# Kernel optimization log

Measured on AMD Instinct MI355X. Metric: run time of the kernel, lower is better.

Reference implementation:

```python
import jax, jax.numpy as jnp
import numpy as np

N = 16384          # nodes
E_R = 524288       # radial edges (avg degree 32)
E_B = 32768        # bonded edges
N_TYPES = 20       # atom types
CS = 64            # scalar (0e) channels
CV = 32            # vector (1o) channels
EA = 16            # edge_attr_dim
EA_B = EA // 2     # bondedness embedding dim
EA_R = (EA + 1) // 2  # radial basis dim
CUTOFF = 1.5       # effective_radial_cutoff
L = 2              # n_layers
NORM = float(np.sqrt((E_R + E_B) / N))  # ~sqrt(avg degree) message normalization


def setup_inputs() -> dict:
    key = jax.random.key(0)
    ks = jax.random.split(key, 32)
    def rn(i, shape, scale=1.0):
        return jax.random.normal(ks[i], shape, dtype=jnp.float32) * scale
    s_e = 1.0 / np.sqrt(EA)
    inp = {}
    inp["pos"] = rn(0, (N, 3))
    inp["c_noise"] = rn(1, (1,))
    inp["atom_types"] = jax.random.randint(ks[2], (N,), 0, N_TYPES)
    inp["radial_edge_index"] = jax.random.randint(ks[3], (2, E_R), 0, N)
    inp["bonded_edge_index"] = jax.random.randint(ks[4], (2, E_B), 0, N)
    # learned parameters
    inp["atom_tab"] = rn(5, (N_TYPES, CS))
    inp["bond_tab"] = rn(6, (2, EA_B))
    inp["ns0_w"] = rn(7, (CS,), 0.1)
    inp["We0"] = rn(8, (EA, CS), s_e)
    inp["We1"] = rn(9, (EA, CS), s_e)
    inp["Wself0"] = rn(10, (CS, CS), 1.0 / np.sqrt(CS))
    inp["Ws0"] = rn(11, (CS, CS), 1.0 / np.sqrt(CS))
    inp["Wv0"] = rn(12, (CS, CV), 1.0 / np.sqrt(CS))
    inp["ns_w"] = rn(13, (L, CS + CV), 0.1)
    inp["We_ss"] = rn(14, (L, EA, CS), s_e)
    inp["We_vs"] = rn(15, (L, EA, CV), s_e)
    inp["We_sv"] = rn(16, (L, EA, CS), s_e)
    inp["We_vv"] = rn(17, (L, EA, CV), s_e)
    inp["We_vx"] = rn(18, (L, EA, CV), s_e)
    inp["Wmix_s"] = rn(19, (L, CS + CV, CS), 1.0 / np.sqrt(CS + CV))
    inp["Wmix_v"] = rn(20, (L, CS + 2 * CV, CV), 1.0 / np.sqrt(CS + 2 * CV))
    inp["Wself_s"] = rn(21, (L, CS, CS), 1.0 / np.sqrt(CS))
    inp["Wself_v"] = rn(22, (L, CV, CV), 1.0 / np.sqrt(CV))
    inp["skip_w"] = rn(23, (L, 2 * (CS + CV)), 0.1)
    inp["skip_b"] = rn(24, (L, 2 * (CS + CV)), 0.1)
    inp["w_out"] = rn(25, (CV,), 1.0 / np.sqrt(CV))
    inp["gain"] = jnp.asarray(0.5, dtype=jnp.float32)
    return inp


def _radial_basis(d):
    # e3nn soft_one_hot_linspace, basis='gaussian', cutoff=True
    centers = jnp.linspace(0.0, CUTOFF, EA_R + 2)[1:-1]
    step = centers[1] - centers[0]
    diff = (d[:, None] - centers[None, :]) / step
    return jnp.exp(-diff * diff) * 1.12


def reference(pos, c_noise, atom_tab, bond_tab, ns0_w, We0, We1, Wself0, Ws0, Wv0,
              ns_w, We_ss, We_vs, We_sv, We_vv, We_vx, Wmix_s, Wmix_v, Wself_s, Wself_v,
              skip_w, skip_b, w_out, gain, atom_types, radial_edge_index, bonded_edge_index):
    edge_index = jnp.concatenate([radial_edge_index, bonded_edge_index], axis=1)
    bond_mask = jnp.concatenate([jnp.zeros((E_R,), jnp.int32), jnp.ones((E_B,), jnp.int32)])
    src, dst = edge_index[0], edge_index[1]
    edge_vec = pos[src] - pos[dst]                      # [E,3]
    d = jnp.sqrt(jnp.sum(edge_vec * edge_vec, -1) + 1e-12)
    Y1 = jnp.sqrt(3.0) * edge_vec / d[:, None]          # l=1 SH, component norm; Y0 == 1
    edge_attr = jnp.concatenate([bond_tab[bond_mask], _radial_basis(d)], axis=-1)  # [E,EA]

    # atom embedding + initial noise-conditional scaling
    s = atom_tab[atom_types] * (1.0 + c_noise * ns0_w)  # [N,CS]

    # initial projector: scalar-input equivariant conv -> hidden irreps
    w0 = edge_attr @ We0
    w1 = edge_attr @ We1
    s_src = s[src]
    a_s = jax.ops.segment_sum(w0 * s_src, dst, num_segments=N) / NORM
    a_v = jax.ops.segment_sum((w1 * s_src)[:, :, None] * Y1[:, None, :], dst, num_segments=N) / NORM
    s_h = a_s @ Ws0 + s @ Wself0                        # [N,CS]
    v_h = jnp.einsum('nci,cd->ndi', a_v, Wv0)           # [N,CV,3]

    for l in range(L):
        # noise-conditional scaling (per-irrep-channel scalar scale)
        scale = 1.0 + c_noise * ns_w[l]
        ss = s_h * scale[:CS]
        vv = v_h * scale[CS:][None, :, None]
        ss_e = ss[src]
        vv_e = vv[src]
        # edge-attr-conditioned tensor-product weights
        w_ss = edge_attr @ We_ss[l]
        w_vs = edge_attr @ We_vs[l]
        w_sv = edge_attr @ We_sv[l]
        w_vv = edge_attr @ We_vv[l]
        w_vx = edge_attr @ We_vx[l]
        # CG tensor-product messages: 0x0->0, 1x1->0 (dot), 0x1->1, 1x0->1, 1x1->1 (cross)
        vdot = jnp.einsum('eci,ei->ec', vv_e, Y1)
        m_s = jnp.concatenate([w_ss * ss_e, w_vs * vdot], axis=-1)          # [E,CS+CV]
        m_v = jnp.concatenate([
            (w_sv * ss_e)[:, :, None] * Y1[:, None, :],
            w_vv[:, :, None] * vv_e,
            w_vx[:, :, None] * jnp.cross(vv_e, Y1[:, None, :]),
        ], axis=1)                                                          # [E,CS+2CV,3]
        a_s = jax.ops.segment_sum(m_s, dst, num_segments=N) / NORM
        a_v = jax.ops.segment_sum(m_v, dst, num_segments=N) / NORM
        new_s = a_s @ Wmix_s[l] + ss @ Wself_s[l]
        new_v = jnp.einsum('nci,cd->ndi', a_v, Wmix_v[l]) + jnp.einsum('nci,cd->ndi', vv, Wself_v[l])
        # noise-conditional skip connection (gated residual)
        g = jax.nn.sigmoid(skip_b[l] + c_noise * skip_w[l])
        s_h = g[:CS] * s_h + g[CS:2 * CS] * new_s
        g_v = g[2 * CS:]
        v_h = g_v[:CV][None, :, None] * v_h + g_v[CV:][None, :, None] * new_v

    # output head: 1o vectors -> 3D displacement, times output gain
    return jnp.einsum('nci,c->ni', v_h, w_out) * gain
```

## Files before the change

kernel.cpp:

```cpp
#include <hip/hip_runtime.h>
#include <math.h>

#define NA 16384
#define ER 524288
#define EB 32768
#define ET 557056
#define INV_NORM 0.17149858514250882f
#define SQRT3 1.7320508075688772f
#define RB_STEP (1.5f/9.0f)
#define BINS 512
#define DMAX 2.5f
#define INV_H ((float)BINS / DMAX)
#define T0U (2 * BINS * 128)
#define TLU (2 * BINS * 256)

typedef unsigned int uint32;
typedef unsigned short ushort16;
typedef float vf4 __attribute__((ext_vector_type(4)));
typedef float vf2 __attribute__((ext_vector_type(2)));
typedef unsigned int vu2 __attribute__((ext_vector_type(2)));

__device__ __forceinline__ float sigmoidf_(float x) { return 1.f / (1.f + __expf(-x)); }

__device__ __forceinline__ ushort16 f2bf(float x) {
  uint32 u = __float_as_uint(x);
  u = u + 0x7FFFu + ((u >> 16) & 1u);
  return (ushort16)(u >> 16);
}
__device__ __forceinline__ uint32 packbf(float hi, float lo) {
  return ((uint32)f2bf(hi) << 16) | (uint32)f2bf(lo);
}
__device__ __forceinline__ float bfhi(uint32 u) { return __uint_as_float(u & 0xFFFF0000u); }
__device__ __forceinline__ float bflo(uint32 u) { return __uint_as_float(u << 16); }

__device__ __forceinline__ float4 ntl4(const float* p) {
  vf4 v = __builtin_nontemporal_load((const vf4*)p);
  return make_float4(v.x, v.y, v.z, v.w);
}
__device__ __forceinline__ float2 ntl2(const float* p) {
  vf2 v = __builtin_nontemporal_load((const vf2*)p);
  return make_float2(v.x, v.y);
}
__device__ __forceinline__ void nts4(float* p, float a, float b, float c, float d) {
  vf4 v; v.x = a; v.y = b; v.z = c; v.w = d;
  __builtin_nontemporal_store(v, (vf4*)p);
}
__device__ __forceinline__ void nts2(float* p, float a, float b) {
  vf2 v; v.x = a; v.y = b;
  __builtin_nontemporal_store(v, (vf2*)p);
}
__device__ __forceinline__ void ntsu2(uint32* p, uint32 a, uint32 b) {
  vu2 v; v.x = a; v.y = b;
  __builtin_nontemporal_store(v, (vu2*)p);
}
__device__ __forceinline__ void nts1(float* p, float a) {
  __builtin_nontemporal_store(a, p);
}

__global__ void k_hist(const int* __restrict__ rad, const int* __restrict__ bon, int* __restrict__ count) {
  int e = blockIdx.x * 256 + threadIdx.x;
  int d = (e < ER) ? rad[ER + e] : bon[EB + (e - ER)];
  atomicAdd(&count[d], 1);
}

__global__ void k_scan1(const int* __restrict__ count, int* __restrict__ partial) {
  __shared__ int red[256];
  int b = blockIdx.x, t = threadIdx.x;
  red[t] = count[b * 256 + t];
  __syncthreads();
  for (int s = 128; s > 0; s >>= 1) {
    if (t < s) red[t] += red[t + s];
    __syncthreads();
  }
  if (t == 0) partial[b] = red[0];
}

__global__ void k_scan2(int* __restrict__ partial) {
  int run = 0;
  for (int i = 0; i < 64; ++i) { int c = partial[i]; partial[i] = run; run += c; }
}

__global__ void k_scan3(const int* __restrict__ count, const int* __restrict__ partial,
                        int* __restrict__ offsets, int* __restrict__ cursor) {
  __shared__ int sc[256];
  int b = blockIdx.x, t = threadIdx.x;
  int v = count[b * 256 + t];
  sc[t] = v;
  __syncthreads();
  for (int off = 1; off < 256; off <<= 1) {
    int x = (t >= off) ? sc[t - off] : 0;
    __syncthreads();
    sc[t] += x;
    __syncthreads();
  }
  int excl = sc[t] - v + partial[b];
  offsets[b * 256 + t] = excl;
  cursor[b * 256 + t] = excl;
  if (b == 63 && t == 255) offsets[NA] = excl + v;
}

__global__ void k_fill_embed(const int* __restrict__ rad, const int* __restrict__ bon,
                             int* __restrict__ cursor, const float* __restrict__ pos,
                             float* __restrict__ rec8,
                             const float* __restrict__ atom_tab, const int* __restrict__ types,
                             const float* __restrict__ ns0_w, const float* __restrict__ cnoise,
                             float* __restrict__ s_feat, ushort16* __restrict__ s_bf) {
  if (blockIdx.x < ET / 256) {
    int e = blockIdx.x * 256 + threadIdx.x;
    int src, dst, v;
    if (e < ER) { src = rad[e]; dst = rad[ER + e]; v = 0; }
    else        { src = bon[e - ER]; dst = bon[EB + e - ER]; v = 1; }
    float dx = pos[src * 3] - pos[dst * 3];
    float dy = pos[src * 3 + 1] - pos[dst * 3 + 1];
    float dz = pos[src * 3 + 2] - pos[dst * 3 + 2];
    float dist = sqrtf(dx * dx + dy * dy + dz * dz + 1e-12f);
    float inv = 1.f / dist;
    float fq = fminf(dist * INV_H, BINS - 1.001f);
    int q = (int)fq;
    float frac = fq - (float)q;
    int qoffL = (v * BINS + q) << 8;
    int slot = atomicAdd(&cursor[dst], 1);
    float* rp = rec8 + (size_t)slot * 8;
    nts4(rp, __int_as_float(src), SQRT3 * dx * inv, SQRT3 * dy * inv, SQRT3 * dz * inv);
    nts2(rp + 4, frac, __int_as_float(qoffL));
  } else {
    int tid = (blockIdx.x - ET / 256) * 256 + threadIdx.x;
    int n = tid >> 6, c = tid & 63;
    float cn = cnoise[0];
    float v = atom_tab[types[n] * 64 + c] * (1.f + cn * ns0_w[c]);
    s_feat[tid] = v;
    s_bf[tid] = f2bf(v);
  }
}

__global__ void k_build(const float* __restrict__ We0, const float* __restrict__ We1,
                        const float* __restrict__ We_ss, const float* __restrict__ We_vs,
                        const float* __restrict__ We_sv, const float* __restrict__ We_vv,
                        const float* __restrict__ We_vx, const float* __restrict__ bond_tab,
                        uint32* __restrict__ T0, uint32* __restrict__ TL) {
  int q = blockIdx.x, t = blockIdx.y, v = blockIdx.z, c = threadIdx.x;
  float d0 = q * (DMAX / BINS), d1 = (q + 1) * (DMAX / BINS);
  float rb0[8], rb1[8];
#pragma unroll
  for (int k = 0; k < 8; ++k) {
    float f0 = (d0 - (k + 1) * RB_STEP) * (1.f / RB_STEP);
    float f1 = (d1 - (k + 1) * RB_STEP) * (1.f / RB_STEP);
    rb0[k] = 1.12f * __expf(-f0 * f0);
    rb1[k] = 1.12f * __expf(-f1 * f1);
  }
  if (t == 0) {
    float ba = 0, bb = 0, a0 = 0, a1 = 0, b0 = 0, b1 = 0;
#pragma unroll
    for (int k = 0; k < 8; ++k) {
      float bt = bond_tab[v * 8 + k];
      float av_lo = We0[k * 64 + c], av_hi = We0[(8 + k) * 64 + c];
      float bv_lo = We1[k * 64 + c], bv_hi = We1[(8 + k) * 64 + c];
      ba += bt * av_lo; bb += bt * bv_lo;
      a0 += rb0[k] * av_hi; a1 += rb1[k] * av_hi;
      b0 += rb0[k] * bv_hi; b1 += rb1[k] * bv_hi;
    }
    uint32* o = T0 + (((size_t)v * BINS + q) << 7) + c * 2;
    o[0] = packbf(ba + a0, a1 - a0);
    o[1] = packbf(bb + b0, b1 - b0);
  } else {
    int l = t - 1;
    const float* Wss = We_ss + l * 1024;
    const float* Wsv = We_sv + l * 1024;
    const float* WA = (c < 32) ? (We_vs + l * 512) : (We_vx + l * 512);
    const float* WB = (c < 32) ? (We_vv + l * 512) : nullptr;
    int cu = c & 31;
    float sa = 0, sb = 0, s0 = 0, s1 = 0, t0 = 0, t1 = 0;
    float ua = 0, ub = 0, u0 = 0, u1 = 0, w0 = 0, w1 = 0;
#pragma unroll
    for (int k = 0; k < 8; ++k) {
      float bt = bond_tab[v * 8 + k];
      float ss_lo = Wss[k * 64 + c], ss_hi = Wss[(8 + k) * 64 + c];
      float sv_lo = Wsv[k * 64 + c], sv_hi = Wsv[(8 + k) * 64 + c];
      sa += bt * ss_lo; sb += bt * sv_lo;
      s0 += rb0[k] * ss_hi; s1 += rb1[k] * ss_hi;
      t0 += rb0[k] * sv_hi; t1 += rb1[k] * sv_hi;
      float a_lo = WA[k * 32 + cu], a_hi = WA[(8 + k) * 32 + cu];
      ua += bt * a_lo;
      u0 += rb0[k] * a_hi; u1 += rb1[k] * a_hi;
      if (WB) {
        float b_lo = WB[k * 32 + cu], b_hi = WB[(8 + k) * 32 + cu];
        ub += bt * b_lo;
        w0 += rb0[k] * b_hi; w1 += rb1[k] * b_hi;
      }
    }
    uint32* o = TL + (size_t)l * TLU + (((size_t)v * BINS + q) << 8) + c * 4;
    o[0] = packbf(sa + s0, s1 - s0);
    o[1] = packbf(sb + t0, t1 - t0);
    o[2] = packbf(ua + u0, u1 - u0);
    o[3] = WB ? packbf(ub + w0, w1 - w0) : 0u;
  }
}

__global__ __launch_bounds__(256, 8) void k_agg0(
    const int* __restrict__ offsets, const float* __restrict__ rec8,
    const uint32* __restrict__ T0, const ushort16* __restrict__ s_bf,
    float* __restrict__ a_s, uint32* __restrict__ a_v) {
  int lane = threadIdx.x & 63;
  int n = blockIdx.x * 4 + (threadIdx.x >> 6);
  float acc = 0, a0 = 0, a1 = 0, a2 = 0;
  int beg = __builtin_amdgcn_readfirstlane(offsets[n]);
  int end = __builtin_amdgcn_readfirstlane(offsets[n + 1]);
  if (beg < end) {
    int last = end - 1;
    int e1 = (beg + 1 < end) ? beg + 1 : last;
    int e2 = (beg + 2 < end) ? beg + 2 : last;
    const float* p0 = rec8 + (size_t)beg * 8;
    const float* p1 = rec8 + (size_t)e1 * 8;
    const float* p2 = rec8 + (size_t)e2 * 8;
    float4 rA0 = ntl4(p0); float2 rB0 = ntl2(p0 + 4);
    float4 rA1 = ntl4(p1); float2 rB1 = ntl2(p1 + 4);
    float4 rA2 = ntl4(p2); float2 rB2 = ntl2(p2 + 4);
    uint2 t0 = *(const uint2*)(T0 + (__float_as_int(rB0.y) >> 1) + (lane << 1));
    ushort16 s0 = s_bf[((size_t)__float_as_int(rA0.x) << 6) + lane];
    uint2 t1 = *(const uint2*)(T0 + (__float_as_int(rB1.y) >> 1) + (lane << 1));
    ushort16 s1 = s_bf[((size_t)__float_as_int(rA1.x) << 6) + lane];
#pragma unroll 3
    for (int idx = beg; idx < end; ++idx) {
      uint2 t2 = *(const uint2*)(T0 + (__float_as_int(rB2.y) >> 1) + (lane << 1));
      ushort16 s2 = s_bf[((size_t)__float_as_int(rA2.x) << 6) + lane];
      int e3 = (idx + 3 < end) ? idx + 3 : last;
      const float* p3 = rec8 + (size_t)e3 * 8;
      float4 rA3 = ntl4(p3); float2 rB3 = ntl2(p3 + 4);
      float frac = rB0.x;
      float w0 = fmaf(frac, bflo(t0.x), bfhi(t0.x));
      float w1 = fmaf(frac, bflo(t0.y), bfhi(t0.y));
      float sv = __uint_as_float((uint32)s0 << 16);
      acc += w0 * sv;
      float t = w1 * sv;
      a0 += t * rA0.y; a1 += t * rA0.z; a2 += t * rA0.w;
      rA0 = rA1; rB0 = rB1; rA1 = rA2; rB1 = rB2; rA2 = rA3; rB2 = rB3;
      t0 = t1; s0 = s1; t1 = t2; s1 = s2;
    }
  }
  nts1(a_s + n * 64 + lane, acc * INV_NORM);
  ntsu2(a_v + ((size_t)n << 7) + (lane << 1),
        packbf(a0 * INV_NORM, a1 * INV_NORM), packbf(a2 * INV_NORM, 0.f));
}

__global__ __launch_bounds__(256, 8) void k_agg_layer(
    const float* __restrict__ cnoise, const float* __restrict__ nsw,
    const int* __restrict__ offsets, const float* __restrict__ rec8,
    const uint32* __restrict__ TL, const ushort16* __restrict__ sh_bf,
    const uint32* __restrict__ vh_bf,
    float* __restrict__ a_s, uint32* __restrict__ a_v) {
  int lane = threadIdx.x & 63;
  int n = blockIdx.x * 4 + (threadIdx.x >> 6);
  int vc = lane & 31;
  bool low = lane < 32;
  float cn = cnoise[0];
  float scale_s = 1.f + cn * nsw[lane];
  float scale_v = 1.f + cn * nsw[64 + vc];

  float ms = 0;
  float av0 = 0, av1 = 0, av2 = 0;
  float ms2 = 0;
  float b0 = 0, b1 = 0, b2 = 0;
  int beg = __builtin_amdgcn_readfirstlane(offsets[n]);
  int end = __builtin_amdgcn_readfirstlane(offsets[n + 1]);
  if (beg < end) {
    int last = end - 1;
    int e1 = (beg + 1 < end) ? beg + 1 : last;
    int e2 = (beg + 2 < end) ? beg + 2 : last;
    const float* p0 = rec8 + (size_t)beg * 8;
    const float* p1 = rec8 + (size_t)e1 * 8;
    const float* p2 = rec8 + (size_t)e2 * 8;
    float4 rA0 = ntl4(p0); float2 rB0 = ntl2(p0 + 4);
    float4 rA1 = ntl4(p1); float2 rB1 = ntl2(p1 + 4);
    float4 rA2 = ntl4(p2); float2 rB2 = ntl2(p2 + 4);
    uint4 t0 = *(const uint4*)(TL + __float_as_int(rB0.y) + (lane << 2));
    ushort16 s0 = sh_bf[((size_t)__float_as_int(rA0.x) << 6) + lane];
    uint2 v0 = *(const uint2*)(vh_bf + ((size_t)__float_as_int(rA0.x) << 6) + (vc << 1));
    uint4 t1 = *(const uint4*)(TL + __float_as_int(rB1.y) + (lane << 2));
    ushort16 s1 = sh_bf[((size_t)__float_as_int(rA1.x) << 6) + lane];
    uint2 v1 = *(const uint2*)(vh_bf + ((size_t)__float_as_int(rA1.x) << 6) + (vc << 1));
#pragma unroll 3
    for (int idx = beg; idx < end; ++idx) {
      uint4 t2 = *(const uint4*)(TL + __float_as_int(rB2.y) + (lane << 2));
      ushort16 s2 = sh_bf[((size_t)__float_as_int(rA2.x) << 6) + lane];
      uint2 v2 = *(const uint2*)(vh_bf + ((size_t)__float_as_int(rA2.x) << 6) + (vc << 1));
      int e3 = (idx + 3 < end) ? idx + 3 : last;
      const float* p3 = rec8 + (size_t)e3 * 8;
      float4 rA3 = ntl4(p3); float2 rB3 = ntl2(p3 + 4);
      float frac = rB0.x;
      float y0 = rA0.y, y1 = rA0.z, y2 = rA0.w;
      float wS  = fmaf(frac, bflo(t0.x), bfhi(t0.x));
      float wSV = fmaf(frac, bflo(t0.y), bfhi(t0.y));
      float wA  = fmaf(frac, bflo(t0.z), bfhi(t0.z));
      float wB  = fmaf(frac, bflo(t0.w), bfhi(t0.w));
      float ss = __uint_as_float((uint32)s0 << 16);
      float vx = bfhi(v0.x), vy = bflo(v0.x), vz = bfhi(v0.y);
      ms += wS * ss;
      float t = wSV * ss;
      av0 += t * y0; av1 += t * y1; av2 += t * y2;
      float vdot = vx * y0 + vy * y1 + vz * y2;
      ms2 += wA * vdot;
      float cx = vy * y2 - vz * y1;
      float cy = vz * y0 - vx * y2;
      float cz = vx * y1 - vy * y0;
      float m0 = low ? vx : cx;
      float m1 = low ? vy : cy;
      float m2 = low ? vz : cz;
      float wM = low ? wB : wA;
      b0 += wM * m0; b1 += wM * m1; b2 += wM * m2;
      rA0 = rA1; rB0 = rB1; rA1 = rA2; rB1 = rB2; rA2 = rA3; rB2 = rB3;
      t0 = t1; s0 = s1; v0 = v1; t1 = t2; s1 = s2; v1 = v2;
    }
  }
  float fs = scale_s * INV_NORM;
  float fv = scale_v * INV_NORM;
  nts1(a_s + n * 96 + lane, ms * fs);
  uint32* avn = a_v + ((size_t)n << 8);
  ntsu2(avn + (lane << 1), packbf(av0 * fs, av1 * fs), packbf(av2 * fs, 0.f));
  if (low) {
    nts1(a_s + n * 96 + 64 + vc, ms2 * fv);
    ntsu2(avn + ((64 + vc) << 1), packbf(b0 * fv, b1 * fv), packbf(b2 * fv, 0.f));
  } else {
    ntsu2(avn + ((96 + vc) << 1), packbf(b0 * fv, b1 * fv), packbf(b2 * fv, 0.f));
  }
}

__global__ __launch_bounds__(256, 4) void k_init(
    const float* __restrict__ a_s, const float* __restrict__ s_feat,
    const float* __restrict__ Ws0, const float* __restrict__ Wself0,
    const uint32* __restrict__ a_v, const float* __restrict__ Wv0,
    float* __restrict__ sh, ushort16* __restrict__ sh_bf,
    float* __restrict__ vh, uint32* __restrict__ vh_bf) {
  __shared__ float SM[9216];
  int tid = threadIdx.x;
  if (blockIdx.x < NA / 8) {
    float* W1 = SM;
    float* W2 = SM + 4096;
    float* La = SM + 8192;
    float* Lf = SM + 8704;
    for (int i = tid; i < 1024; i += 256) {
      ((float4*)W1)[i] = ((const float4*)Ws0)[i];
      ((float4*)W2)[i] = ((const float4*)Wself0)[i];
    }
    int base = blockIdx.x * 8;
    for (int i = tid; i < 512; i += 256) {
      La[i] = a_s[(size_t)base * 64 + i];
      Lf[i] = s_feat[(size_t)base * 64 + i];
    }
    __syncthreads();
    int d = tid & 63, g = tid >> 6;
    int n0 = base + g * 2;
    const float* A0 = La + g * 128;
    const float* A1 = A0 + 64;
    const float* F0 = Lf + g * 128;
    const float* F1 = F0 + 64;
    float a0 = 0, a1 = 0;
#pragma unroll 8
    for (int c = 0; c < 64; ++c) {
      float w1 = W1[c * 64 + d], w2 = W2[c * 64 + d];
      a0 += A0[c] * w1 + F0[c] * w2;
      a1 += A1[c] * w1 + F1[c] * w2;
    }
    sh[(size_t)n0 * 64 + d] = a0;
    sh[(size_t)(n0 + 1) * 64 + d] = a1;
    sh_bf[(size_t)n0 * 64 + d] = f2bf(a0);
    sh_bf[(size_t)(n0 + 1) * 64 + d] = f2bf(a1);
  } else {
    float* W = SM;
    for (int i = tid; i < 512; i += 256) ((float4*)W)[i] = ((const float4*)Wv0)[i];
    __syncthreads();
    int d = tid & 31, g = tid >> 5;
    int n = (blockIdx.x - NA / 8) * 8 + g;
    const uint2* av = (const uint2*)a_v + ((size_t)n << 6);
    float x = 0, y = 0, z = 0;
#pragma unroll 4
    for (int c = 0; c < 64; ++c) {
      uint2 a = av[c];
      float w = W[c * 32 + d];
      x += bfhi(a.x) * w; y += bflo(a.x) * w; z += bfhi(a.y) * w;
    }
    *(float4*)(vh + ((size_t)n << 7) + (d << 2)) = make_float4(x, y, z, 0.f);
    *(uint2*)(vh_bf + ((size_t)n << 6) + (d << 1)) = make_uint2(packbf(x, y), packbf(z, 0.f));
  }
}

__global__ __launch_bounds__(256, 4) void k_mix(
    const float* __restrict__ a_s, const float* __restrict__ sh_in,
    const float* __restrict__ Wmix_s, const float* __restrict__ Wself_s,
    const uint32* __restrict__ a_v, const float* __restrict__ vh_in,
    const float* __restrict__ Wmix_v, const float* __restrict__ Wself_v,
    const float* __restrict__ nsw, const float* __restrict__ skw,
    const float* __restrict__ skb, const float* __restrict__ cnoise,
    float* __restrict__ sh_out, ushort16* __restrict__ sh_bf_out,
    float* __restrict__ vh_out, uint32* __restrict__ vh_bf_out) {
  __shared__ float SM[11008];
  int tid = threadIdx.x;
  float cn = cnoise[0];
  if (blockIdx.x < NA / 8) {
    float* Wm = SM;
    float* Wsf = SM + 6144;
    float* La = SM + 10240;
    for (int i = tid; i < 96 * 16; i += 256) ((float4*)Wm)[i] = ((const float4*)Wmix_s)[i];
    for (int i = tid; i < 64 * 16; i += 256) {
      float4 wv = ((const float4*)Wself_s)[i];
      int c = i >> 4;
      float sc = 1.f + cn * nsw[c];
      wv.x *= sc; wv.y *= sc; wv.z *= sc; wv.w *= sc;
      ((float4*)Wsf)[i] = wv;
    }
    int base = blockIdx.x * 8;
    for (int i = tid; i < 8 * 96; i += 256) La[i] = a_s[(size_t)base * 96 + i];
    __syncthreads();
    int d = tid & 63, g = tid >> 6;
    int n0 = base + g * 2;
    const float* A0 = La + (g * 2) * 96;
    const float* A1 = A0 + 96;
    const float* s0p = sh_in + (size_t)n0 * 64;
    const float* s1p = s0p + 64;
    float acc0 = 0, acc1 = 0;
#pragma unroll 8
    for (int c = 0; c < 96; ++c) {
      float w = Wm[c * 64 + d];
      acc0 += A0[c] * w;
      acc1 += A1[c] * w;
    }
#pragma unroll 8
    for (int c = 0; c < 64; ++c) {
      float w = Wsf[c * 64 + d];
      acc0 += s0p[c] * w;
      acc1 += s1p[c] * w;
    }
    float g1 = sigmoidf_(skb[d] + cn * skw[d]);
    float g2 = sigmoidf_(skb[64 + d] + cn * skw[64 + d]);
    float o0 = g1 * s0p[d] + g2 * acc0;
    float o1 = g1 * s1p[d] + g2 * acc1;
    sh_out[(size_t)n0 * 64 + d] = o0;
    sh_out[(size_t)(n0 + 1) * 64 + d] = o1;
    sh_bf_out[(size_t)n0 * 64 + d] = f2bf(o0);
    sh_bf_out[(size_t)(n0 + 1) * 64 + d] = f2bf(o1);
  } else {
    float* Wm = SM;
    float* Wsf = SM + 4096;
    for (int i = tid; i < 128 * 8; i += 256) ((float4*)Wm)[i] = ((const float4*)Wmix_v)[i];
    for (int i = tid; i < 32 * 8; i += 256) {
      float4 wv = ((const float4*)Wself_v)[i];
      int c = i >> 3;
      float sc = 1.f + cn * nsw[64 + c];
      wv.x *= sc; wv.y *= sc; wv.z *= sc; wv.w *= sc;
      ((float4*)Wsf)[i] = wv;
    }
    __syncthreads();
    int d = tid & 31, g = tid >> 5;
    int n = (blockIdx.x - NA / 8) * 8 + g;
    const uint2* av = (const uint2*)a_v + ((size_t)n << 7);
    const float4* vr = (const float4*)(vh_in + ((size_t)n << 7));
    float x = 0, y = 0, z = 0;
#pragma unroll 4
    for (int c = 0; c < 128; ++c) {
      uint2 a = av[c];
      float w = Wm[c * 32 + d];
      x += bfhi(a.x) * w; y += bflo(a.x) * w; z += bfhi(a.y) * w;
    }
#pragma unroll 4
    for (int c = 0; c < 32; ++c) {
      float4 vv = vr[c];
      float w = Wsf[c * 32 + d];
      x += vv.x * w; y += vv.y * w; z += vv.z * w;
    }
    float g3 = sigmoidf_(skb[128 + d] + cn * skw[128 + d]);
    float g4 = sigmoidf_(skb[160 + d] + cn * skw[160 + d]);
    float4 vi = vr[d];
    float ox = g3 * vi.x + g4 * x;
    float oy = g3 * vi.y + g4 * y;
    float oz = g3 * vi.z + g4 * z;
    *(float4*)(vh_out + ((size_t)n << 7) + (d << 2)) = make_float4(ox, oy, oz, 0.f);
    *(uint2*)(vh_bf_out + ((size_t)n << 6) + (d << 1)) = make_uint2(packbf(ox, oy), packbf(oz, 0.f));
  }
}

__global__ void k_out(const float* __restrict__ vh, const float* __restrict__ w_out,
                      const float* __restrict__ gain, float* __restrict__ out) {
  int tid = blockIdx.x * 256 + threadIdx.x;
  int n = tid / 3, i = tid - n * 3;
  float acc = 0;
  for (int c = 0; c < 32; ++c) acc += vh[((size_t)n << 7) + c * 4 + i] * w_out[c];
  out[tid] = acc * gain[0];
}

extern "C" void kernel_launch(void* const* d_in, const int* in_sizes, int n_in,
                              void* d_out, int out_size, void* d_ws, size_t ws_size,
                              hipStream_t stream) {
  (void)in_sizes; (void)n_in; (void)out_size; (void)ws_size;
  const float* pos     = (const float*)d_in[0];
  const float* cn      = (const float*)d_in[1];
  const int*   types   = (const int*)d_in[2];
  const int*   rad     = (const int*)d_in[3];
  const int*   bon     = (const int*)d_in[4];
  const float* atom_tab= (const float*)d_in[5];
  const float* bond_tab= (const float*)d_in[6];
  const float* ns0_w   = (const float*)d_in[7];
  const float* We0     = (const float*)d_in[8];
  const float* We1     = (const float*)d_in[9];
  const float* Wself0  = (const float*)d_in[10];
  const float* Ws0     = (const float*)d_in[11];
  const float* Wv0     = (const float*)d_in[12];
  const float* ns_w    = (const float*)d_in[13];
  const float* We_ss   = (const float*)d_in[14];
  const float* We_vs   = (const float*)d_in[15];
  const float* We_sv   = (const float*)d_in[16];
  const float* We_vv   = (const float*)d_in[17];
  const float* We_vx   = (const float*)d_in[18];
  const float* Wmix_s  = (const float*)d_in[19];
  const float* Wmix_v  = (const float*)d_in[20];
  const float* Wself_s = (const float*)d_in[21];
  const float* Wself_v = (const float*)d_in[22];
  const float* skip_w  = (const float*)d_in[23];
  const float* skip_b  = (const float*)d_in[24];
  const float* w_out   = (const float*)d_in[25];
  const float* gain    = (const float*)d_in[26];

  char* ws = (char*)d_ws;
  size_t o = 0;
  auto alloc = [&](size_t bytes) -> void* {
    void* p = ws + o;
    o += (bytes + 255) & ~(size_t)255;
    return p;
  };
  float* s_feat  = (float*)alloc((size_t)NA * 64 * 4);
  ushort16* s_bf = (ushort16*)alloc((size_t)NA * 64 * 2);
  float* a_s     = (float*)alloc((size_t)NA * 96 * 4);
  uint32* a_v    = (uint32*)alloc((size_t)NA * 256 * 4);
  float* sh0     = (float*)alloc((size_t)NA * 64 * 4);
  float* sh1     = (float*)alloc((size_t)NA * 64 * 4);
  ushort16* shbf0= (ushort16*)alloc((size_t)NA * 64 * 2);
  ushort16* shbf1= (ushort16*)alloc((size_t)NA * 64 * 2);
  float* vh0     = (float*)alloc((size_t)NA * 128 * 4);
  float* vh1     = (float*)alloc((size_t)NA * 128 * 4);
  uint32* vhbf0  = (uint32*)alloc((size_t)NA * 64 * 4);
  uint32* vhbf1  = (uint32*)alloc((size_t)NA * 64 * 4);
  int* count     = (int*)alloc((size_t)NA * 4);
  int* partial   = (int*)alloc((size_t)64 * 4);
  int* offsets   = (int*)alloc((size_t)(NA + 1) * 4);
  int* cursor    = (int*)alloc((size_t)NA * 4);
  float* rec8    = (float*)alloc((size_t)ET * 32);
  uint32* T0     = (uint32*)alloc((size_t)T0U * 4);
  uint32* TL     = (uint32*)alloc((size_t)2 * TLU * 4);
  float* shb[2]  = {sh0, sh1};
  ushort16* shbf[2] = {shbf0, shbf1};
  float* vhb[2]  = {vh0, vh1};
  uint32* vhbf[2]= {vhbf0, vhbf1};

  hipMemsetAsync(count, 0, (size_t)NA * 4, stream);
  k_hist<<<ET / 256, 256, 0, stream>>>(rad, bon, count);
  k_scan1<<<64, 256, 0, stream>>>(count, partial);
  k_scan2<<<1, 1, 0, stream>>>(partial);
  k_scan3<<<64, 256, 0, stream>>>(count, partial, offsets, cursor);
  k_fill_embed<<<ET / 256 + NA * 64 / 256, 256, 0, stream>>>(
      rad, bon, cursor, pos, rec8, atom_tab, types, ns0_w, cn, s_feat, s_bf);
  k_build<<<dim3(BINS, 3, 2), 64, 0, stream>>>(We0, We1, We_ss, We_vs, We_sv, We_vv, We_vx,
                                               bond_tab, T0, TL);

  k_agg0<<<NA / 4, 256, 0, stream>>>(offsets, rec8, T0, s_bf, a_s, a_v);
  k_init<<<NA / 4, 256, 0, stream>>>(a_s, s_feat, Ws0, Wself0, a_v, Wv0,
                                     shb[0], shbf[0], vhb[0], vhbf[0]);

  for (int l = 0; l < 2; ++l) {
    int bin = l & 1, bout = 1 - bin;
    k_agg_layer<<<NA / 4, 256, 0, stream>>>(
        cn, ns_w + l * 96, offsets, rec8, TL + (size_t)l * TLU, shbf[bin], vhbf[bin], a_s, a_v);
    k_mix<<<NA / 4, 256, 0, stream>>>(
        a_s, shb[bin], Wmix_s + l * 96 * 64, Wself_s + l * 64 * 64,
        a_v, vhb[bin], Wmix_v + l * 128 * 32, Wself_v + l * 32 * 32,
        ns_w + l * 96, skip_w + l * 192, skip_b + l * 192, cn,
        shb[bout], shbf[bout], vhb[bout], vhbf[bout]);
  }
  k_out<<<NA * 3 / 256, 256, 0, stream>>>(vhb[0], w_out, gain, (float*)d_out);
}
```

Baseline: 508.8 us.

## Split init/mix kernels into scalar and vector kernels with bf16-packed LDS weights

```diff
diff --git a/kernel.cpp b/kernel.cpp
--- a/kernel.cpp
+++ b/kernel.cpp
@@ -324,157 +324,182 @@
   }
 }
 
-__global__ __launch_bounds__(256, 4) void k_init(
+__global__ __launch_bounds__(256, 8) void k_init_s(
     const float* __restrict__ a_s, const float* __restrict__ s_feat,
     const float* __restrict__ Ws0, const float* __restrict__ Wself0,
+    float* __restrict__ sh, ushort16* __restrict__ sh_bf) {
+  __shared__ uint32 W1[32 * 64];
+  __shared__ uint32 W2[32 * 64];
+  __shared__ float La[8 * 64];
+  __shared__ float Lf[8 * 64];
+  int tid = threadIdx.x;
+  for (int i = tid; i < 32 * 64; i += 256) {
+    int k = i >> 6, d = i & 63;
+    W1[i] = packbf(Ws0[(2 * k) * 64 + d], Ws0[(2 * k + 1) * 64 + d]);
+    W2[i] = packbf(Wself0[(2 * k) * 64 + d], Wself0[(2 * k + 1) * 64 + d]);
+  }
+  int base = blockIdx.x * 8;
+  for (int i = tid; i < 512; i += 256) {
+    La[i] = a_s[(size_t)base * 64 + i];
+    Lf[i] = s_feat[(size_t)base * 64 + i];
+  }
+  __syncthreads();
+  int d = tid & 63, g = tid >> 6;
+  int n0 = base + g * 2;
+  const float* A0 = La + g * 128;
+  const float* A1 = A0 + 64;
+  const float* F0 = Lf + g * 128;
+  const float* F1 = F0 + 64;
+  float a0 = 0, a1 = 0;
+#pragma unroll 8
+  for (int k = 0; k < 32; ++k) {
+    uint32 w1 = W1[k * 64 + d], w2 = W2[k * 64 + d];
+    int c = 2 * k;
+    a0 += A0[c] * bfhi(w1) + A0[c + 1] * bflo(w1) + F0[c] * bfhi(w2) + F0[c + 1] * bflo(w2);
+    a1 += A1[c] * bfhi(w1) + A1[c + 1] * bflo(w1) + F1[c] * bfhi(w2) + F1[c + 1] * bflo(w2);
+  }
+  sh[(size_t)n0 * 64 + d] = a0;
+  sh[(size_t)(n0 + 1) * 64 + d] = a1;
+  sh_bf[(size_t)n0 * 64 + d] = f2bf(a0);
+  sh_bf[(size_t)(n0 + 1) * 64 + d] = f2bf(a1);
+}
+
+__global__ __launch_bounds__(256, 8) void k_init_v(
     const uint32* __restrict__ a_v, const float* __restrict__ Wv0,
-    float* __restrict__ sh, ushort16* __restrict__ sh_bf,
     float* __restrict__ vh, uint32* __restrict__ vh_bf) {
-  __shared__ float SM[9216];
+  __shared__ uint32 W[32 * 32];
   int tid = threadIdx.x;
-  if (blockIdx.x < NA / 8) {
-    float* W1 = SM;
-    float* W2 = SM + 4096;
-    float* La = SM + 8192;
-    float* Lf = SM + 8704;
-    for (int i = tid; i < 1024; i += 256) {
-      ((float4*)W1)[i] = ((const float4*)Ws0)[i];
-      ((float4*)W2)[i] = ((const float4*)Wself0)[i];
-    }
-    int base = blockIdx.x * 8;
-    for (int i = tid; i < 512; i += 256) {
-      La[i] = a_s[(size_t)base * 64 + i];
-      Lf[i] = s_feat[(size_t)base * 64 + i];
-    }
-    __syncthreads();
-    int d = tid & 63, g = tid >> 6;
-    int n0 = base + g * 2;
-    const float* A0 = La + g * 128;
-    const float* A1 = A0 + 64;
-    const float* F0 = Lf + g * 128;
-    const float* F1 = F0 + 64;
-    float a0 = 0, a1 = 0;
+  for (int i = tid; i < 32 * 32; i += 256) {
+    int k = i >> 5, d = i & 31;
+    W[i] = packbf(Wv0[(2 * k) * 32 + d], Wv0[(2 * k + 1) * 32 + d]);
+  }
+  __syncthreads();
+  int d = tid & 31, g = tid >> 5;
+  int n = blockIdx.x * 8 + g;
+  const uint2* av = (const uint2*)a_v + ((size_t)n << 6);
+  float x = 0, y = 0, z = 0;
 #pragma unroll 8
-    for (int c = 0; c < 64; ++c) {
-      float w1 = W1[c * 64 + d], w2 = W2[c * 64 + d];
-      a0 += A0[c] * w1 + F0[c] * w2;
-      a1 += A1[c] * w1 + F1[c] * w2;
-    }
-    sh[(size_t)n0 * 64 + d] = a0;
-    sh[(size_t)(n0 + 1) * 64 + d] = a1;
-    sh_bf[(size_t)n0 * 64 + d] = f2bf(a0);
-    sh_bf[(size_t)(n0 + 1) * 64 + d] = f2bf(a1);
-  } else {
-    float* W = SM;
-    for (int i = tid; i < 512; i += 256) ((float4*)W)[i] = ((const float4*)Wv0)[i];
-    __syncthreads();
-    int d = tid & 31, g = tid >> 5;
-    int n = (blockIdx.x - NA / 8) * 8 + g;
-    const uint2* av = (const uint2*)a_v + ((size_t)n << 6);
-    float x = 0, y = 0, z = 0;
-#pragma unroll 4
-    for (int c = 0; c < 64; ++c) {
-      uint2 a = av[c];
-      float w = W[c * 32 + d];
-      x += bfhi(a.x) * w; y += bflo(a.x) * w; z += bfhi(a.y) * w;
-    }
-    *(float4*)(vh + ((size_t)n << 7) + (d << 2)) = make_float4(x, y, z, 0.f);
-    *(uint2*)(vh_bf + ((size_t)n << 6) + (d << 1)) = make_uint2(packbf(x, y), packbf(z, 0.f));
-  }
-}
-
-__global__ __launch_bounds__(256, 4) void k_mix(
+  for (int k = 0; k < 32; ++k) {
+    uint32 w = W[k * 32 + d];
+    uint2 e0 = av[2 * k], e1 = av[2 * k + 1];
+    float w0 = bfhi(w), w1 = bflo(w);
+    x += bfhi(e0.x) * w0 + bfhi(e1.x) * w1;
+    y += bflo(e0.x) * w0 + bflo(e1.x) * w1;
+    z += bfhi(e0.y) * w0 + bfhi(e1.y) * w1;
+  }
+  *(float4*)(vh + ((size_t)n << 7) + (d << 2)) = make_float4(x, y, z, 0.f);
+  *(uint2*)(vh_bf + ((size_t)n << 6) + (d << 1)) = make_uint2(packbf(x, y), packbf(z, 0.f));
+}
+
+__global__ __launch_bounds__(256, 6) void k_mix_s(
     const float* __restrict__ a_s, const float* __restrict__ sh_in,
     const float* __restrict__ Wmix_s, const float* __restrict__ Wself_s,
+    const float* __restrict__ nsw, const float* __restrict__ skw,
+    const float* __restrict__ skb, const float* __restrict__ cnoise,
+    float* __restrict__ sh_out, ushort16* __restrict__ sh_bf_out) {
+  __shared__ uint32 Wm[48 * 64];
+  __shared__ uint32 Wsf[32 * 64];
+  __shared__ float La[8 * 96];
+  int tid = threadIdx.x;
+  float cn = cnoise[0];
+  for (int i = tid; i < 48 * 64; i += 256) {
+    int k = i >> 6, d = i & 63;
+    Wm[i] = packbf(Wmix_s[(2 * k) * 64 + d], Wmix_s[(2 * k + 1) * 64 + d]);
+  }
+  for (int i = tid; i < 32 * 64; i += 256) {
+    int k = i >> 6, d = i & 63;
+    float sc0 = 1.f + cn * nsw[2 * k];
+    float sc1 = 1.f + cn * nsw[2 * k + 1];
+    Wsf[i] = packbf(Wself_s[(2 * k) * 64 + d] * sc0, Wself_s[(2 * k + 1) * 64 + d] * sc1);
+  }
+  int base = blockIdx.x * 8;
+  for (int i = tid; i < 8 * 96; i += 256) La[i] = a_s[(size_t)base * 96 + i];
+  __syncthreads();
+  int d = tid & 63, g = tid >> 6;
+  int n0 = base + g * 2;
+  const float* A0 = La + (g * 2) * 96;
+  const float* A1 = A0 + 96;
+  const float* s0p = sh_in + (size_t)n0 * 64;
+  const float* s1p = s0p + 64;
+  float acc0 = 0, acc1 = 0;
+#pragma unroll 8
+  for (int k = 0; k < 48; ++k) {
+    uint32 w = Wm[k * 64 + d];
+    int c = 2 * k;
+    float wh = bfhi(w), wl = bflo(w);
+    acc0 += A0[c] * wh + A0[c + 1] * wl;
+    acc1 += A1[c] * wh + A1[c + 1] * wl;
+  }
+#pragma unroll 8
+  for (int k = 0; k < 32; ++k) {
+    uint32 w = Wsf[k * 64 + d];
+    int c = 2 * k;
+    float wh = bfhi(w), wl = bflo(w);
+    acc0 += s0p[c] * wh + s0p[c + 1] * wl;
+    acc1 += s1p[c] * wh + s1p[c + 1] * wl;
+  }
+  float g1 = sigmoidf_(skb[d] + cn * skw[d]);
+  float g2 = sigmoidf_(skb[64 + d] + cn * skw[64 + d]);
+  float o0 = g1 * s0p[d] + g2 * acc0;
+  float o1 = g1 * s1p[d] + g2 * acc1;
+  sh_out[(size_t)n0 * 64 + d] = o0;
+  sh_out[(size_t)(n0 + 1) * 64 + d] = o1;
+  sh_bf_out[(size_t)n0 * 64 + d] = f2bf(o0);
+  sh_bf_out[(size_t)(n0 + 1) * 64 + d] = f2bf(o1);
+}
+
+__global__ __launch_bounds__(256, 8) void k_mix_v(
     const uint32* __restrict__ a_v, const float* __restrict__ vh_in,
     const float* __restrict__ Wmix_v, const float* __restrict__ Wself_v,
     const float* __restrict__ nsw, const float* __restrict__ skw,
     const float* __restrict__ skb, const float* __restrict__ cnoise,
-    float* __restrict__ sh_out, ushort16* __restrict__ sh_bf_out,
     float* __restrict__ vh_out, uint32* __restrict__ vh_bf_out) {
-  __shared__ float SM[11008];
+  __shared__ uint32 Wm[64 * 32];
+  __shared__ uint32 Wsf[16 * 32];
   int tid = threadIdx.x;
   float cn = cnoise[0];
-  if (blockIdx.x < NA / 8) {
-    float* Wm = SM;
-    float* Wsf = SM + 6144;
-    float* La = SM + 10240;
-    for (int i = tid; i < 96 * 16; i += 256) ((float4*)Wm)[i] = ((const float4*)Wmix_s)[i];
-    for (int i = tid; i < 64 * 16; i += 256) {
-      float4 wv = ((const float4*)Wself_s)[i];
-      int c = i >> 4;
-      float sc = 1.f + cn * nsw[c];
-      wv.x *= sc; wv.y *= sc; wv.z *= sc; wv.w *= sc;
-      ((float4*)Wsf)[i] = wv;
-    }
-    int base = blockIdx.x * 8;
-    for (int i = tid; i < 8 * 96; i += 256) La[i] = a_s[(size_t)base * 96 + i];
-    __syncthreads();
-    int d = tid & 63, g = tid >> 6;
-    int n0 = base + g * 2;
-    const float* A0 = La + (g * 2) * 96;
-    const float* A1 = A0 + 96;
-    const float* s0p = sh_in + (size_t)n0 * 64;
-    const float* s1p = s0p + 64;
-    float acc0 = 0, acc1 = 0;
+  for (int i = tid; i < 64 * 32; i += 256) {
+    int k = i >> 5, d = i & 31;
+    Wm[i] = packbf(Wmix_v[(2 * k) * 32 + d], Wmix_v[(2 * k + 1) * 32 + d]);
+  }
+  for (int i = tid; i < 16 * 32; i += 256) {
+    int k = i >> 5, d = i & 31;
+    float sc0 = 1.f + cn * nsw[64 + 2 * k];
+    float sc1 = 1.f + cn * nsw[64 + 2 * k + 1];
+    Wsf[i] = packbf(Wself_v[(2 * k) * 32 + d] * sc0, Wself_v[(2 * k + 1) * 32 + d] * sc1);
+  }
+  __syncthreads();
+  int d = tid & 31, g = tid >> 5;
+  int n = blockIdx.x * 8 + g;
+  const uint2* av = (const uint2*)a_v + ((size_t)n << 7);
+  const float4* vr = (const float4*)(vh_in + ((size_t)n << 7));
+  float x = 0, y = 0, z = 0;
 #pragma unroll 8
-    for (int c = 0; c < 96; ++c) {
-      float w = Wm[c * 64 + d];
-      acc0 += A0[c] * w;
-      acc1 += A1[c] * w;
-    }
+  for (int k = 0; k < 64; ++k) {
+    uint32 w = Wm[k * 32 + d];
+    uint2 e0 = av[2 * k], e1 = av[2 * k + 1];
+    float w0 = bfhi(w), w1 = bflo(w);
+    x += bfhi(e0.x) * w0 + bfhi(e1.x) * w1;
+    y += bflo(e0.x) * w0 + bflo(e1.x) * w1;
+    z += bfhi(e0.y) * w0 + bfhi(e1.y) * w1;
+  }
 #pragma unroll 8
-    for (int c = 0; c < 64; ++c) {
-      float w = Wsf[c * 64 + d];
-      acc0 += s0p[c] * w;
-      acc1 += s1p[c] * w;
-    }
-    float g1 = sigmoidf_(skb[d] + cn * skw[d]);
-    float g2 = sigmoidf_(skb[64 + d] + cn * skw[64 + d]);
-    float o0 = g1 * s0p[d] + g2 * acc0;
-    float o1 = g1 * s1p[d] + g2 * acc1;
-    sh_out[(size_t)n0 * 64 + d] = o0;
-    sh_out[(size_t)(n0 + 1) * 64 + d] = o1;
-    sh_bf_out[(size_t)n0 * 64 + d] = f2bf(o0);
-    sh_bf_out[(size_t)(n0 + 1) * 64 + d] = f2bf(o1);
-  } else {
-    float* Wm = SM;
-    float* Wsf = SM + 4096;
-    for (int i = tid; i < 128 * 8; i += 256) ((float4*)Wm)[i] = ((const float4*)Wmix_v)[i];
-    for (int i = tid; i < 32 * 8; i += 256) {
-      float4 wv = ((const float4*)Wself_v)[i];
-      int c = i >> 3;
-      float sc = 1.f + cn * nsw[64 + c];
-      wv.x *= sc; wv.y *= sc; wv.z *= sc; wv.w *= sc;
-      ((float4*)Wsf)[i] = wv;
-    }
-    __syncthreads();
-    int d = tid & 31, g = tid >> 5;
-    int n = (blockIdx.x - NA / 8) * 8 + g;
-    const uint2* av = (const uint2*)a_v + ((size_t)n << 7);
-    const float4* vr = (const float4*)(vh_in + ((size_t)n << 7));
-    float x = 0, y = 0, z = 0;
-#pragma unroll 4
-    for (int c = 0; c < 128; ++c) {
-      uint2 a = av[c];
-      float w = Wm[c * 32 + d];
-      x += bfhi(a.x) * w; y += bflo(a.x) * w; z += bfhi(a.y) * w;
-    }
-#pragma unroll 4
-    for (int c = 0; c < 32; ++c) {
-      float4 vv = vr[c];
-      float w = Wsf[c * 32 + d];
-      x += vv.x * w; y += vv.y * w; z += vv.z * w;
-    }
-    float g3 = sigmoidf_(skb[128 + d] + cn * skw[128 + d]);
-    float g4 = sigmoidf_(skb[160 + d] + cn * skw[160 + d]);
-    float4 vi = vr[d];
-    float ox = g3 * vi.x + g4 * x;
-    float oy = g3 * vi.y + g4 * y;
-    float oz = g3 * vi.z + g4 * z;
-    *(float4*)(vh_out + ((size_t)n << 7) + (d << 2)) = make_float4(ox, oy, oz, 0.f);
-    *(uint2*)(vh_bf_out + ((size_t)n << 6) + (d << 1)) = make_uint2(packbf(ox, oy), packbf(oz, 0.f));
-  }
+  for (int k = 0; k < 16; ++k) {
+    uint32 w = Wsf[k * 32 + d];
+    float4 e0 = vr[2 * k], e1 = vr[2 * k + 1];
+    float w0 = bfhi(w), w1 = bflo(w);
+    x += e0.x * w0 + e1.x * w1;
+    y += e0.y * w0 + e1.y * w1;
+    z += e0.z * w0 + e1.z * w1;
+  }
+  float g3 = sigmoidf_(skb[128 + d] + cn * skw[128 + d]);
+  float g4 = sigmoidf_(skb[160 + d] + cn * skw[160 + d]);
+  float4 vi = vr[d];
+  float ox = g3 * vi.x + g4 * x;
+  float oy = g3 * vi.y + g4 * y;
+  float oz = g3 * vi.z + g4 * z;
+  *(float4*)(vh_out + ((size_t)n << 7) + (d << 2)) = make_float4(ox, oy, oz, 0.f);
+  *(uint2*)(vh_bf_out + ((size_t)n << 6) + (d << 1)) = make_uint2(packbf(ox, oy), packbf(oz, 0.f));
 }
 
 __global__ void k_out(const float* __restrict__ vh, const float* __restrict__ w_out,
@@ -560,18 +585,19 @@
                                                bond_tab, T0, TL);
 
   k_agg0<<<NA / 4, 256, 0, stream>>>(offsets, rec8, T0, s_bf, a_s, a_v);
-  k_init<<<NA / 4, 256, 0, stream>>>(a_s, s_feat, Ws0, Wself0, a_v, Wv0,
-                                     shb[0], shbf[0], vhb[0], vhbf[0]);
+  k_init_s<<<NA / 8, 256, 0, stream>>>(a_s, s_feat, Ws0, Wself0, shb[0], shbf[0]);
+  k_init_v<<<NA / 8, 256, 0, stream>>>(a_v, Wv0, vhb[0], vhbf[0]);
 
   for (int l = 0; l < 2; ++l) {
     int bin = l & 1, bout = 1 - bin;
     k_agg_layer<<<NA / 4, 256, 0, stream>>>(
         cn, ns_w + l * 96, offsets, rec8, TL + (size_t)l * TLU, shbf[bin], vhbf[bin], a_s, a_v);
-    k_mix<<<NA / 4, 256, 0, stream>>>(
+    k_mix_s<<<NA / 8, 256, 0, stream>>>(
         a_s, shb[bin], Wmix_s + l * 96 * 64, Wself_s + l * 64 * 64,
+        ns_w + l * 96, skip_w + l * 192, skip_b + l * 192, cn, shb[bout], shbf[bout]);
+    k_mix_v<<<NA / 8, 256, 0, stream>>>(
         a_v, vhb[bin], Wmix_v + l * 128 * 32, Wself_v + l * 32 * 32,
-        ns_w + l * 96, skip_w + l * 192, skip_b + l * 192, cn,
-        shb[bout], shbf[bout], vhb[bout], vhbf[bout]);
+        ns_w + l * 96, skip_w + l * 192, skip_b + l * 192, cn, vhb[bout], vhbf[bout]);
   }
   k_out<<<NA * 3 / 256, 256, 0, stream>>>(vhb[0], w_out, gain, (float*)d_out);
 }
```

Measured after the change: 503.2 us. Within noise of the previous version (-1.1%).
